# Kernel tuning notes

Measured on AMD Instinct MI355X. Metric: run time of the kernel, lower is better.

## Reference

```python
import jax, jax.numpy as jnp
import numpy as np

B, S, D = 1, 4096, 1024
H, W = 16, 512            # heads, window_size
HD = D // H               # head_dim = 64


def setup_inputs() -> dict:
    key = jax.random.key(0)
    k1, k2, k3 = jax.random.split(key, 3)
    x = jax.random.normal(k1, (B, S, D), dtype=jnp.float32)
    w_qkv = jax.random.normal(k2, (D, 3 * D), dtype=jnp.float32) * 0.02
    w_out = jax.random.normal(k3, (D, D), dtype=jnp.float32) * 0.02
    return {"x": x, "w_qkv": w_qkv, "w_out": w_out}


def reference(x, w_qkv, w_out):
    b, s, d = x.shape
    qkv = x @ w_qkv                                   # [B,S,3D]
    q, k, v = jnp.split(qkv, 3, axis=-1)
    to_heads = lambda t: t.reshape(b, s, H, HD).transpose(0, 2, 1, 3)  # [B,H,S,hd]
    q, k, v = map(to_heads, (q, k, v))

    C = s // W                                        # number of chunks
    qc = q.reshape(b, H, C, W, HD)                    # [B,H,C,W,hd]
    kc = k.reshape(b, H, C, W, HD)
    vc = v.reshape(b, H, C, W, HD)

    # each chunk attends to [previous chunk, current chunk] of K/V (2W keys)
    zero = jnp.zeros_like(kc[:, :, :1])
    k_prev = jnp.concatenate([zero, kc[:, :, :-1]], axis=2)
    v_prev = jnp.concatenate([jnp.zeros_like(vc[:, :, :1]), vc[:, :, :-1]], axis=2)
    kcat = jnp.concatenate([k_prev, kc], axis=3)      # [B,H,C,2W,hd]
    vcat = jnp.concatenate([v_prev, vc], axis=3)

    scores = jnp.einsum('bhcqd,bhckd->bhcqk', qc, kcat) / (HD ** 0.5)

    # mask: causal (abs q_pos >= abs k_pos) and k_pos >= 0 (first chunk has no prev)
    wq = jnp.arange(W)
    jk = jnp.arange(2 * W)
    ci = jnp.arange(C)
    causal = (wq[:, None] + W) >= jk[None, :]                    # [W,2W]
    valid = (ci[:, None, None] * W + jk[None, None, :] - W) >= 0  # [C,1,2W]
    mask = causal[None] & valid                                   # [C,W,2W]

    scores = jnp.where(mask[None, None], scores, -jnp.inf)
    attn = jax.nn.softmax(scores, axis=-1)
    out = jnp.einsum('bhcqk,bhckd->bhcqd', attn, vcat)            # [B,H,C,W,hd]
    out = out.reshape(b, H, s, HD).transpose(0, 2, 1, 3).reshape(b, s, d)
    return out @ w_out
```

## Files before the change

### kernel.cpp

```cpp
#include <hip/hip_runtime.h>

typedef __attribute__((ext_vector_type(8))) short short8;
typedef __attribute__((ext_vector_type(4))) float f32x4;
typedef __attribute__((ext_vector_type(4))) unsigned short us4;
typedef unsigned short u16;

__device__ __forceinline__ u16 f2bf(float f) {
  unsigned int u = __float_as_uint(f);
  u += 0x7fffu + ((u >> 16) & 1u);
  return (u16)(u >> 16);
}

__device__ __forceinline__ void gld16(const void* g, void* l) {
  __builtin_amdgcn_global_load_lds((const __attribute__((address_space(1))) void*)g,
                                   (__attribute__((address_space(3))) void*)l, 16, 0, 0);
}

__global__ __launch_bounds__(256) void cast_f32_to_bf16(const float* __restrict__ in,
                                                        u16* __restrict__ out, int n8) {
  int i = blockIdx.x * 256 + threadIdx.x;
  if (i >= n8) return;
  const f32x4* p = (const f32x4*)in;
  f32x4 a = p[i * 2];
  f32x4 b = p[i * 2 + 1];
  short8 o;
#pragma unroll
  for (int j = 0; j < 4; ++j) o[j] = (short)f2bf(a[j]);
#pragma unroll
  for (int j = 0; j < 4; ++j) o[4 + j] = (short)f2bf(b[j]);
  ((short8*)out)[i] = o;
}

__global__ __launch_bounds__(256) void transpose_cast(const float* __restrict__ w,
                                                      u16* __restrict__ wT, int K, int N) {
  __shared__ float tile[32][33];
  int n0 = blockIdx.x * 32, k0 = blockIdx.y * 32;
  int r = threadIdx.x >> 5;
  int c = threadIdx.x & 31;
#pragma unroll
  for (int i = 0; i < 4; ++i)
    tile[r + i * 8][c] = w[(size_t)(k0 + r + i * 8) * N + n0 + c];
  __syncthreads();
#pragma unroll
  for (int i = 0; i < 4; ++i)
    wT[(size_t)(n0 + r + i * 8) * K + k0 + c] = f2bf(tile[c][r + i * 8]);
}

__global__ __launch_bounds__(256) void transpose_v(const u16* __restrict__ vh,
                                                   u16* __restrict__ vt) {
  __shared__ u16 tile[32][33];
  const int s0 = blockIdx.x * 32, d0 = blockIdx.y * 32, h = blockIdx.z;
  const long hb = (long)h * 4096 * 64;
  const long hb2 = (long)h * 64 * 4096;
  const int r = threadIdx.x >> 5, c = threadIdx.x & 31;
#pragma unroll
  for (int i = 0; i < 4; ++i)
    tile[r + i * 8][c] = vh[hb + (long)(s0 + r + i * 8) * 64 + d0 + c];
  __syncthreads();
#pragma unroll
  for (int i = 0; i < 4; ++i)
    vt[hb2 + (long)(d0 + r + i * 8) * 4096 + s0 + c] = tile[c][r + i * 8];
}

template <int MODE, int BN>
__global__ __launch_bounds__(256) void gemm_bf16(
    const u16* __restrict__ A, const u16* __restrict__ Bt, float* __restrict__ C,
    u16* __restrict__ q_out, u16* __restrict__ k_out, u16* __restrict__ v_out,
    int M, int N, int K) {
  __shared__ __align__(16) u16 As[128][64];
  __shared__ __align__(16) u16 Bs[BN][64];
  constexpr int NW = BN / 32;
  const int t = threadIdx.x;
  const int lane = t & 63;
  const int wid = t >> 6;
  const int wm = wid >> 1, wn = wid & 1;
  const int l15 = lane & 15, lhi = lane >> 4;

  const int nbx = gridDim.x;
  const int bid = blockIdx.y * nbx + blockIdx.x;
  const int cpx = (nbx * gridDim.y) >> 3;
  const int wg = (bid & 7) * cpx + (bid >> 3);
  const int m0 = (wg / nbx) * 128;
  const int n0 = (wg % nbx) * BN;

  const int srow = lane >> 3;
  const int scol = ((lane & 7) ^ (lane >> 3)) * 8;

  f32x4 acc[4][NW];
#pragma unroll
  for (int mi = 0; mi < 4; ++mi)
#pragma unroll
    for (int ni = 0; ni < NW; ++ni) acc[mi][ni] = (f32x4){0.f, 0.f, 0.f, 0.f};

  for (int k0 = 0; k0 < K; k0 += 64) {
    __syncthreads();
#pragma unroll
    for (int i = 0; i < 4; ++i) {
      int cch = wid * 4 + i;
      int row = cch * 8 + srow;
      const u16* src = (MODE == 2)
          ? &A[((size_t)(k0 >> 6) * 4096 + m0 + row) * 64 + scol]
          : &A[(size_t)(m0 + row) * K + k0 + scol];
      gld16(src, &As[cch * 8][0]);
    }
#pragma unroll
    for (int i = 0; i < NW; ++i) {
      int cch = wid * NW + i;
      int row = cch * 8 + srow;
      gld16(&Bt[(size_t)(n0 + row) * K + k0 + scol], &Bs[cch * 8][0]);
    }
    __syncthreads();
#pragma unroll
    for (int kc = 0; kc < 2; ++kc) {
      short8 af[4], bf[NW];
#pragma unroll
      for (int mi = 0; mi < 4; ++mi) {
        int row = wm * 64 + mi * 16 + l15;
        af[mi] = *(const short8*)&As[row][((kc * 4 + lhi) ^ (l15 & 7)) * 8];
      }
#pragma unroll
      for (int ni = 0; ni < NW; ++ni) {
        int row = wn * (BN / 2) + ni * 16 + l15;
        bf[ni] = *(const short8*)&Bs[row][((kc * 4 + lhi) ^ (l15 & 7)) * 8];
      }
#pragma unroll
      for (int mi = 0; mi < 4; ++mi)
#pragma unroll
        for (int ni = 0; ni < NW; ++ni)
          acc[mi][ni] = __builtin_amdgcn_mfma_f32_16x16x32_bf16(af[mi], bf[ni], acc[mi][ni], 0, 0, 0);
    }
  }

  const float SCQ = 0.18033688011112042f;
#pragma unroll
  for (int mi = 0; mi < 4; ++mi)
#pragma unroll
    for (int ni = 0; ni < NW; ++ni)
#pragma unroll
      for (int r = 0; r < 4; ++r) {
        int row = m0 + wm * 64 + mi * 16 + lhi * 4 + r;
        int col = n0 + wn * (BN / 2) + ni * 16 + l15;
        float val = acc[mi][ni][r];
        if constexpr (MODE == 1) {
          int which = col >> 10;
          int d = col & 1023;
          int hh = d >> 6, hd = d & 63;
          if (which == 0)      q_out[((size_t)hh * 4096 + row) * 64 + hd] = f2bf(val * SCQ);
          else if (which == 1) k_out[((size_t)hh * 4096 + row) * 64 + hd] = f2bf(val);
          else                 v_out[((size_t)hh * 4096 + row) * 64 + hd] = f2bf(val);
        } else {
          C[(size_t)row * N + col] = val;
        }
      }
}

__global__ __launch_bounds__(256) void attn_kernel(
    const u16* __restrict__ qh,
    const u16* __restrict__ kh,
    const u16* __restrict__ vt,
    u16* __restrict__ outh) {
  __shared__ __align__(16) u16 Ks[2][64][64];
  __shared__ __align__(16) u16 Vt[2][64][64];
  __shared__ __align__(16) unsigned int Pl[4][32][37];

  const int t = threadIdx.x;
  const int lane = t & 63;
  const int w = t >> 6;
  const int l15 = lane & 15;
  const int lhi = lane >> 4;

  const int bid = blockIdx.x;
  const int wk = (bid & 7) * 64 + (bid >> 3);
  const int qt = wk & 3, c = (wk >> 2) & 7, h = wk >> 5;

  const long head_base = (long)h * 4096 * 64;
  const int q0 = qt * 128;
  const long q_gbase = head_base + (long)(c * 512 + q0) * 64;

  short8 qf[2][2];
#pragma unroll
  for (int mi = 0; mi < 2; ++mi)
#pragma unroll
    for (int kc = 0; kc < 2; ++kc)
      qf[mi][kc] = *(const short8*)&qh[q_gbase + (long)(w * 32 + mi * 16 + l15) * 64 + kc * 32 + lhi * 8];

  float m_run[2] = {-1e30f, -1e30f}, l_run[2] = {0.f, 0.f};
  f32x4 acc_o[2][4];
#pragma unroll
  for (int mi = 0; mi < 2; ++mi)
#pragma unroll
    for (int nd = 0; nd < 4; ++nd) acc_o[mi][nd] = (f32x4){0.f, 0.f, 0.f, 0.f};

  const int kt_start = (c == 0) ? 8 : 0;
  const int kt_end = 2 * qt + 9;
  const long kv_base = head_base + ((long)c - 1) * 512 * 64;
  const long vt_hb = (long)h * 64 * 4096 + ((long)c - 1) * 512;

  const int srow = lane >> 3;
  const int sunit8 = ((lane & 7) ^ (lane >> 3)) * 8;

  {
    const int j0 = kt_start * 64;
#pragma unroll
    for (int i = 0; i < 2; ++i) {
      int cch = w * 2 + i;
      gld16(&kh[kv_base + (long)(j0 + cch * 8 + srow) * 64 + sunit8], &Ks[0][cch * 8][0]);
      gld16(&vt[vt_hb + (long)(cch * 8 + srow) * 4096 + j0 + sunit8], &Vt[0][cch * 8][0]);
    }
  }
  __syncthreads();

  int cur = 0;
  for (int kt = kt_start; kt <= kt_end; ++kt) {
    const int j0 = kt * 64;
    const int nxt = cur ^ 1;

    if (kt < kt_end) {
      const int j0n = j0 + 64;
#pragma unroll
      for (int i = 0; i < 2; ++i) {
        int cch = w * 2 + i;
        gld16(&kh[kv_base + (long)(j0n + cch * 8 + srow) * 64 + sunit8], &Ks[nxt][cch * 8][0]);
        gld16(&vt[vt_hb + (long)(cch * 8 + srow) * 4096 + j0n + sunit8], &Vt[nxt][cch * 8][0]);
      }
    }

    const bool active = (j0 <= q0 + w * 32 + 31 + 512);
    if (active) {
      f32x4 sa[2][4];
#pragma unroll
      for (int mi = 0; mi < 2; ++mi)
#pragma unroll
        for (int ni = 0; ni < 4; ++ni) sa[mi][ni] = (f32x4){0.f, 0.f, 0.f, 0.f};
#pragma unroll
      for (int kc = 0; kc < 2; ++kc) {
        short8 kf[4];
#pragma unroll
        for (int ni = 0; ni < 4; ++ni) {
          int row = ni * 16 + l15;
          kf[ni] = *(const short8*)&Ks[cur][row][((kc * 4 + lhi) ^ (l15 & 7)) * 8];
        }
#pragma unroll
        for (int mi = 0; mi < 2; ++mi)
#pragma unroll
          for (int ni = 0; ni < 4; ++ni)
            sa[mi][ni] = __builtin_amdgcn_mfma_f32_16x16x32_bf16(kf[ni], qf[mi][kc], sa[mi][ni], 0, 0, 0);
      }

      const bool need_mask = (j0 + 63 > q0 + w * 32 + 512);
#pragma unroll
      for (int mi = 0; mi < 2; ++mi) {
        const int qloc = q0 + w * 32 + mi * 16 + l15;
        if (need_mask) {
          const int lim = qloc + 512 - j0 - 4 * lhi;
#pragma unroll
          for (int ni = 0; ni < 4; ++ni)
#pragma unroll
            for (int r = 0; r < 4; ++r)
              if (16 * ni + r > lim) sa[mi][ni][r] = -1e30f;
        }
        float v[16];
#pragma unroll
        for (int ni = 0; ni < 4; ++ni)
#pragma unroll
          for (int r = 0; r < 4; ++r) v[ni * 4 + r] = sa[mi][ni][r];
#pragma unroll
        for (int s = 8; s >= 1; s >>= 1)
#pragma unroll
          for (int k = 0; k < s; ++k) v[k] = fmaxf(v[k], v[k + s]);
        float tm = v[0];
        tm = fmaxf(tm, __shfl_xor(tm, 16, 64));
        tm = fmaxf(tm, __shfl_xor(tm, 32, 64));

        float mn = fmaxf(m_run[mi], tm);
        float corr = __builtin_amdgcn_exp2f(m_run[mi] - mn);
        m_run[mi] = mn;

        float ps[16];
#pragma unroll
        for (int ni = 0; ni < 4; ++ni) {
#pragma unroll
          for (int r = 0; r < 4; ++r) ps[ni * 4 + r] = __builtin_amdgcn_exp2f(sa[mi][ni][r] - mn);
          unsigned int p01 = (unsigned int)f2bf(ps[ni * 4 + 0]) | ((unsigned int)f2bf(ps[ni * 4 + 1]) << 16);
          unsigned int p23 = (unsigned int)f2bf(ps[ni * 4 + 2]) | ((unsigned int)f2bf(ps[ni * 4 + 3]) << 16);
          Pl[w][mi * 16 + l15][8 * ni + 2 * lhi + 0] = p01;
          Pl[w][mi * 16 + l15][8 * ni + 2 * lhi + 1] = p23;
        }
#pragma unroll
        for (int s = 8; s >= 1; s >>= 1)
#pragma unroll
          for (int k = 0; k < s; ++k) ps[k] += ps[k + s];
        float ls = ps[0];
        ls += __shfl_xor(ls, 16, 64);
        ls += __shfl_xor(ls, 32, 64);
        l_run[mi] = l_run[mi] * corr + ls;
#pragma unroll
        for (int nd = 0; nd < 4; ++nd)
#pragma unroll
          for (int r = 0; r < 4; ++r) acc_o[mi][nd][r] *= corr;
      }

#pragma unroll
      for (int kc = 0; kc < 2; ++kc) {
        short8 pf[2];
#pragma unroll
        for (int mi = 0; mi < 2; ++mi)
          pf[mi] = *(const short8*)&Pl[w][mi * 16 + l15][kc * 16 + lhi * 4];
#pragma unroll
        for (int nd = 0; nd < 4; ++nd) {
          int row = nd * 16 + l15;
          short8 vf = *(const short8*)&Vt[cur][row][((kc * 4 + lhi) ^ (l15 & 7)) * 8];
#pragma unroll
          for (int mi = 0; mi < 2; ++mi)
            acc_o[mi][nd] = __builtin_amdgcn_mfma_f32_16x16x32_bf16(vf, pf[mi], acc_o[mi][nd], 0, 0, 0);
        }
      }
    }
    __syncthreads();
    cur = nxt;
  }

#pragma unroll
  for (int mi = 0; mi < 2; ++mi) {
    float inv = 1.f / l_run[mi];
    long s = (long)c * 512 + q0 + w * 32 + mi * 16 + l15;
#pragma unroll
    for (int nd = 0; nd < 4; ++nd) {
      us4 o;
#pragma unroll
      for (int r = 0; r < 4; ++r) o[r] = f2bf(acc_o[mi][nd][r] * inv);
      *(us4*)&outh[head_base + s * 64 + nd * 16 + lhi * 4] = o;
    }
  }
}

extern "C" void kernel_launch(void* const* d_in, const int* in_sizes, int n_in,
                              void* d_out, int out_size, void* d_ws, size_t ws_size,
                              hipStream_t stream) {
  const float* x = (const float*)d_in[0];
  const float* w_qkv = (const float*)d_in[1];
  const float* w_out = (const float*)d_in[2];
  float* out = (float*)d_out;

  u16* xb = (u16*)d_ws;
  u16* wqkvT = xb + 4096 * 1024;
  u16* woutT = wqkvT + 3072 * 1024;
  u16* qh = woutT + 1024 * 1024;
  u16* kh = qh + 16 * 4096 * 64;
  u16* vh = kh + 16 * 4096 * 64;
  u16* vt = xb;

  cast_f32_to_bf16<<<2048, 256, 0, stream>>>(x, xb, 4096 * 1024 / 8);
  transpose_cast<<<dim3(96, 32), 256, 0, stream>>>(w_qkv, wqkvT, 1024, 3072);
  transpose_cast<<<dim3(32, 32), 256, 0, stream>>>(w_out, woutT, 1024, 1024);

  gemm_bf16<1, 128><<<dim3(24, 32), 256, 0, stream>>>(xb, wqkvT, nullptr, qh, kh, vh,
                                                      4096, 3072, 1024);
  transpose_v<<<dim3(128, 2, 16), 256, 0, stream>>>(vh, vt);
  attn_kernel<<<512, 256, 0, stream>>>(qh, kh, vt, qh);
  gemm_bf16<2, 64><<<dim3(16, 32), 256, 0, stream>>>(qh, woutT, out, nullptr, nullptr, nullptr,
                                                     4096, 1024, 1024);
}
```

Before: 182.5 us.

## Use 8 waves per attention block and smaller output GEMM tiles

The attention kernel now runs 512 threads per block, with each wave owning 16 query rows instead of 32. K/V tile loads are split across 8 waves, so each wave issues one load per tile instead of two. The output projection GEMM is templated on BM and uses 64x64 tiles, doubling the grid to fill more CUs. This lowers per-wave register pressure and raises parallelism, at the cost of less reuse of K/V fragments per MFMA and more per-wave softmax overhead.

```diff
diff --git a/kernel.cpp b/kernel.cpp
--- a/kernel.cpp
+++ b/kernel.cpp
@@ -62,13 +62,14 @@
     vt[hb2 + (long)(d0 + r + i * 8) * 4096 + s0 + c] = tile[c][r + i * 8];
 }
 
-template <int MODE, int BN>
+template <int MODE, int BM, int BN>
 __global__ __launch_bounds__(256) void gemm_bf16(
     const u16* __restrict__ A, const u16* __restrict__ Bt, float* __restrict__ C,
     u16* __restrict__ q_out, u16* __restrict__ k_out, u16* __restrict__ v_out,
     int M, int N, int K) {
-  __shared__ __align__(16) u16 As[128][64];
+  __shared__ __align__(16) u16 As[BM][64];
   __shared__ __align__(16) u16 Bs[BN][64];
+  constexpr int MW = BM / 32;
   constexpr int NW = BN / 32;
   const int t = threadIdx.x;
   const int lane = t & 63;
@@ -80,23 +81,23 @@
   const int bid = blockIdx.y * nbx + blockIdx.x;
   const int cpx = (nbx * gridDim.y) >> 3;
   const int wg = (bid & 7) * cpx + (bid >> 3);
-  const int m0 = (wg / nbx) * 128;
+  const int m0 = (wg / nbx) * BM;
   const int n0 = (wg % nbx) * BN;
 
   const int srow = lane >> 3;
   const int scol = ((lane & 7) ^ (lane >> 3)) * 8;
 
-  f32x4 acc[4][NW];
-#pragma unroll
-  for (int mi = 0; mi < 4; ++mi)
+  f32x4 acc[MW][NW];
+#pragma unroll
+  for (int mi = 0; mi < MW; ++mi)
 #pragma unroll
     for (int ni = 0; ni < NW; ++ni) acc[mi][ni] = (f32x4){0.f, 0.f, 0.f, 0.f};
 
   for (int k0 = 0; k0 < K; k0 += 64) {
     __syncthreads();
 #pragma unroll
-    for (int i = 0; i < 4; ++i) {
-      int cch = wid * 4 + i;
+    for (int i = 0; i < MW; ++i) {
+      int cch = wid * MW + i;
       int row = cch * 8 + srow;
       const u16* src = (MODE == 2)
           ? &A[((size_t)(k0 >> 6) * 4096 + m0 + row) * 64 + scol]
@@ -112,10 +113,10 @@
     __syncthreads();
 #pragma unroll
     for (int kc = 0; kc < 2; ++kc) {
-      short8 af[4], bf[NW];
-#pragma unroll
-      for (int mi = 0; mi < 4; ++mi) {
-        int row = wm * 64 + mi * 16 + l15;
+      short8 af[MW], bf[NW];
+#pragma unroll
+      for (int mi = 0; mi < MW; ++mi) {
+        int row = wm * (BM / 2) + mi * 16 + l15;
         af[mi] = *(const short8*)&As[row][((kc * 4 + lhi) ^ (l15 & 7)) * 8];
       }
 #pragma unroll
@@ -124,7 +125,7 @@
         bf[ni] = *(const short8*)&Bs[row][((kc * 4 + lhi) ^ (l15 & 7)) * 8];
       }
 #pragma unroll
-      for (int mi = 0; mi < 4; ++mi)
+      for (int mi = 0; mi < MW; ++mi)
 #pragma unroll
         for (int ni = 0; ni < NW; ++ni)
           acc[mi][ni] = __builtin_amdgcn_mfma_f32_16x16x32_bf16(af[mi], bf[ni], acc[mi][ni], 0, 0, 0);
@@ -133,12 +134,12 @@
 
   const float SCQ = 0.18033688011112042f;
 #pragma unroll
-  for (int mi = 0; mi < 4; ++mi)
+  for (int mi = 0; mi < MW; ++mi)
 #pragma unroll
     for (int ni = 0; ni < NW; ++ni)
 #pragma unroll
       for (int r = 0; r < 4; ++r) {
-        int row = m0 + wm * 64 + mi * 16 + lhi * 4 + r;
+        int row = m0 + wm * (BM / 2) + mi * 16 + lhi * 4 + r;
         int col = n0 + wn * (BN / 2) + ni * 16 + l15;
         float val = acc[mi][ni][r];
         if constexpr (MODE == 1) {
@@ -154,14 +155,14 @@
       }
 }
 
-__global__ __launch_bounds__(256) void attn_kernel(
+__global__ __launch_bounds__(512) void attn_kernel(
     const u16* __restrict__ qh,
     const u16* __restrict__ kh,
     const u16* __restrict__ vt,
     u16* __restrict__ outh) {
   __shared__ __align__(16) u16 Ks[2][64][64];
   __shared__ __align__(16) u16 Vt[2][64][64];
-  __shared__ __align__(16) unsigned int Pl[4][32][37];
+  __shared__ __align__(16) unsigned int Pl[8][16][37];
 
   const int t = threadIdx.x;
   const int lane = t & 63;
@@ -177,19 +178,15 @@
   const int q0 = qt * 128;
   const long q_gbase = head_base + (long)(c * 512 + q0) * 64;
 
-  short8 qf[2][2];
-#pragma unroll
-  for (int mi = 0; mi < 2; ++mi)
-#pragma unroll
-    for (int kc = 0; kc < 2; ++kc)
-      qf[mi][kc] = *(const short8*)&qh[q_gbase + (long)(w * 32 + mi * 16 + l15) * 64 + kc * 32 + lhi * 8];
-
-  float m_run[2] = {-1e30f, -1e30f}, l_run[2] = {0.f, 0.f};
-  f32x4 acc_o[2][4];
-#pragma unroll
-  for (int mi = 0; mi < 2; ++mi)
-#pragma unroll
-    for (int nd = 0; nd < 4; ++nd) acc_o[mi][nd] = (f32x4){0.f, 0.f, 0.f, 0.f};
+  short8 qf[2];
+#pragma unroll
+  for (int kc = 0; kc < 2; ++kc)
+    qf[kc] = *(const short8*)&qh[q_gbase + (long)(w * 16 + l15) * 64 + kc * 32 + lhi * 8];
+
+  float m_run = -1e30f, l_run = 0.f;
+  f32x4 acc_o[4];
+#pragma unroll
+  for (int nd = 0; nd < 4; ++nd) acc_o[nd] = (f32x4){0.f, 0.f, 0.f, 0.f};
 
   const int kt_start = (c == 0) ? 8 : 0;
   const int kt_end = 2 * qt + 9;
@@ -201,12 +198,8 @@
 
   {
     const int j0 = kt_start * 64;
-#pragma unroll
-    for (int i = 0; i < 2; ++i) {
-      int cch = w * 2 + i;
-      gld16(&kh[kv_base + (long)(j0 + cch * 8 + srow) * 64 + sunit8], &Ks[0][cch * 8][0]);
-      gld16(&vt[vt_hb + (long)(cch * 8 + srow) * 4096 + j0 + sunit8], &Vt[0][cch * 8][0]);
-    }
+    gld16(&kh[kv_base + (long)(j0 + w * 8 + srow) * 64 + sunit8], &Ks[0][w * 8][0]);
+    gld16(&vt[vt_hb + (long)(w * 8 + srow) * 4096 + j0 + sunit8], &Vt[0][w * 8][0]);
   }
   __syncthreads();
 
@@ -217,21 +210,15 @@
 
     if (kt < kt_end) {
       const int j0n = j0 + 64;
-#pragma unroll
-      for (int i = 0; i < 2; ++i) {
-        int cch = w * 2 + i;
-        gld16(&kh[kv_base + (long)(j0n + cch * 8 + srow) * 64 + sunit8], &Ks[nxt][cch * 8][0]);
-        gld16(&vt[vt_hb + (long)(cch * 8 + srow) * 4096 + j0n + sunit8], &Vt[nxt][cch * 8][0]);
-      }
-    }
-
-    const bool active = (j0 <= q0 + w * 32 + 31 + 512);
+      gld16(&kh[kv_base + (long)(j0n + w * 8 + srow) * 64 + sunit8], &Ks[nxt][w * 8][0]);
+      gld16(&vt[vt_hb + (long)(w * 8 + srow) * 4096 + j0n + sunit8], &Vt[nxt][w * 8][0]);
+    }
+
+    const bool active = (j0 <= q0 + w * 16 + 15 + 512);
     if (active) {
-      f32x4 sa[2][4];
-#pragma unroll
-      for (int mi = 0; mi < 2; ++mi)
-#pragma unroll
-        for (int ni = 0; ni < 4; ++ni) sa[mi][ni] = (f32x4){0.f, 0.f, 0.f, 0.f};
+      f32x4 sa[4];
+#pragma unroll
+      for (int ni = 0; ni < 4; ++ni) sa[ni] = (f32x4){0.f, 0.f, 0.f, 0.f};
 #pragma unroll
       for (int kc = 0; kc < 2; ++kc) {
         short8 kf[4];
@@ -241,78 +228,67 @@
           kf[ni] = *(const short8*)&Ks[cur][row][((kc * 4 + lhi) ^ (l15 & 7)) * 8];
         }
 #pragma unroll
-        for (int mi = 0; mi < 2; ++mi)
-#pragma unroll
-          for (int ni = 0; ni < 4; ++ni)
-            sa[mi][ni] = __builtin_amdgcn_mfma_f32_16x16x32_bf16(kf[ni], qf[mi][kc], sa[mi][ni], 0, 0, 0);
-      }
-
-      const bool need_mask = (j0 + 63 > q0 + w * 32 + 512);
-#pragma unroll
-      for (int mi = 0; mi < 2; ++mi) {
-        const int qloc = q0 + w * 32 + mi * 16 + l15;
-        if (need_mask) {
-          const int lim = qloc + 512 - j0 - 4 * lhi;
-#pragma unroll
-          for (int ni = 0; ni < 4; ++ni)
-#pragma unroll
-            for (int r = 0; r < 4; ++r)
-              if (16 * ni + r > lim) sa[mi][ni][r] = -1e30f;
-        }
-        float v[16];
-#pragma unroll
         for (int ni = 0; ni < 4; ++ni)
-#pragma unroll
-          for (int r = 0; r < 4; ++r) v[ni * 4 + r] = sa[mi][ni][r];
-#pragma unroll
-        for (int s = 8; s >= 1; s >>= 1)
-#pragma unroll
-          for (int k = 0; k < s; ++k) v[k] = fmaxf(v[k], v[k + s]);
-        float tm = v[0];
-        tm = fmaxf(tm, __shfl_xor(tm, 16, 64));
-        tm = fmaxf(tm, __shfl_xor(tm, 32, 64));
-
-        float mn = fmaxf(m_run[mi], tm);
-        float corr = __builtin_amdgcn_exp2f(m_run[mi] - mn);
-        m_run[mi] = mn;
-
-        float ps[16];
-#pragma unroll
-        for (int ni = 0; ni < 4; ++ni) {
-#pragma unroll
-          for (int r = 0; r < 4; ++r) ps[ni * 4 + r] = __builtin_amdgcn_exp2f(sa[mi][ni][r] - mn);
-          unsigned int p01 = (unsigned int)f2bf(ps[ni * 4 + 0]) | ((unsigned int)f2bf(ps[ni * 4 + 1]) << 16);
-          unsigned int p23 = (unsigned int)f2bf(ps[ni * 4 + 2]) | ((unsigned int)f2bf(ps[ni * 4 + 3]) << 16);
-          Pl[w][mi * 16 + l15][8 * ni + 2 * lhi + 0] = p01;
-          Pl[w][mi * 16 + l15][8 * ni + 2 * lhi + 1] = p23;
-        }
-#pragma unroll
-        for (int s = 8; s >= 1; s >>= 1)
-#pragma unroll
-          for (int k = 0; k < s; ++k) ps[k] += ps[k + s];
-        float ls = ps[0];
-        ls += __shfl_xor(ls, 16, 64);
-        ls += __shfl_xor(ls, 32, 64);
-        l_run[mi] = l_run[mi] * corr + ls;
-#pragma unroll
-        for (int nd = 0; nd < 4; ++nd)
-#pragma unroll
-          for (int r = 0; r < 4; ++r) acc_o[mi][nd][r] *= corr;
-      }
+          sa[ni] = __builtin_amdgcn_mfma_f32_16x16x32_bf16(kf[ni], qf[kc], sa[ni], 0, 0, 0);
+      }
+
+      const int qloc = q0 + w * 16 + l15;
+      if (j0 + 63 > q0 + w * 16 + 512) {
+        const int lim = qloc + 512 - j0 - 4 * lhi;
+#pragma unroll
+        for (int ni = 0; ni < 4; ++ni)
+#pragma unroll
+          for (int r = 0; r < 4; ++r)
+            if (16 * ni + r > lim) sa[ni][r] = -1e30f;
+      }
+      float v[16];
+#pragma unroll
+      for (int ni = 0; ni < 4; ++ni)
+#pragma unroll
+        for (int r = 0; r < 4; ++r) v[ni * 4 + r] = sa[ni][r];
+#pragma unroll
+      for (int s = 8; s >= 1; s >>= 1)
+#pragma unroll
+        for (int k = 0; k < s; ++k) v[k] = fmaxf(v[k], v[k + s]);
+      float tm = v[0];
+      tm = fmaxf(tm, __shfl_xor(tm, 16, 64));
+      tm = fmaxf(tm, __shfl_xor(tm, 32, 64));
+
+      float mn = fmaxf(m_run, tm);
+      float corr = __builtin_amdgcn_exp2f(m_run - mn);
+      m_run = mn;
+
+      float ps[16];
+#pragma unroll
+      for (int ni = 0; ni < 4; ++ni) {
+#pragma unroll
+        for (int r = 0; r < 4; ++r) ps[ni * 4 + r] = __builtin_amdgcn_exp2f(sa[ni][r] - mn);
+        unsigned int p01 = (unsigned int)f2bf(ps[ni * 4 + 0]) | ((unsigned int)f2bf(ps[ni * 4 + 1]) << 16);
+        unsigned int p23 = (unsigned int)f2bf(ps[ni * 4 + 2]) | ((unsigned int)f2bf(ps[ni * 4 + 3]) << 16);
+        Pl[w][l15][8 * ni + 2 * lhi + 0] = p01;
+        Pl[w][l15][8 * ni + 2 * lhi + 1] = p23;
+      }
+#pragma unroll
+      for (int s = 8; s >= 1; s >>= 1)
+#pragma unroll
+        for (int k = 0; k < s; ++k) ps[k] += ps[k + s];
+      float ls = ps[0];
+      ls += __shfl_xor(ls, 16, 64);
+      ls += __shfl_xor(ls, 32, 64);
+      l_run = l_run * corr + ls;
+#pragma unroll
+      for (int nd = 0; nd < 4; ++nd)
+#pragma unroll
+        for (int r = 0; r < 4; ++r) acc_o[nd][r] *= corr;
 
 #pragma unroll
       for (int kc = 0; kc < 2; ++kc) {
-        short8 pf[2];
-#pragma unroll
-        for (int mi = 0; mi < 2; ++mi)
-          pf[mi] = *(const short8*)&Pl[w][mi * 16 + l15][kc * 16 + lhi * 4];
+        short8 pf = *(const short8*)&Pl[w][l15][kc * 16 + lhi * 4];
 #pragma unroll
         for (int nd = 0; nd < 4; ++nd) {
           int row = nd * 16 + l15;
           short8 vf = *(const short8*)&Vt[cur][row][((kc * 4 + lhi) ^ (l15 & 7)) * 8];
-#pragma unroll
-          for (int mi = 0; mi < 2; ++mi)
-            acc_o[mi][nd] = __builtin_amdgcn_mfma_f32_16x16x32_bf16(vf, pf[mi], acc_o[mi][nd], 0, 0, 0);
+          acc_o[nd] = __builtin_amdgcn_mfma_f32_16x16x32_bf16(vf, pf, acc_o[nd], 0, 0, 0);
         }
       }
     }
@@ -320,15 +296,14 @@
     cur = nxt;
   }
 
-#pragma unroll
-  for (int mi = 0; mi < 2; ++mi) {
-    float inv = 1.f / l_run[mi];
-    long s = (long)c * 512 + q0 + w * 32 + mi * 16 + l15;
+  {
+    float inv = 1.f / l_run;
+    long s = (long)c * 512 + q0 + w * 16 + l15;
 #pragma unroll
     for (int nd = 0; nd < 4; ++nd) {
       us4 o;
 #pragma unroll
-      for (int r = 0; r < 4; ++r) o[r] = f2bf(acc_o[mi][nd][r] * inv);
+      for (int r = 0; r < 4; ++r) o[r] = f2bf(acc_o[nd][r] * inv);
       *(us4*)&outh[head_base + s * 64 + nd * 16 + lhi * 4] = o;
     }
   }
@@ -354,10 +329,10 @@
   transpose_cast<<<dim3(96, 32), 256, 0, stream>>>(w_qkv, wqkvT, 1024, 3072);
   transpose_cast<<<dim3(32, 32), 256, 0, stream>>>(w_out, woutT, 1024, 1024);
 
-  gemm_bf16<1, 128><<<dim3(24, 32), 256, 0, stream>>>(xb, wqkvT, nullptr, qh, kh, vh,
-                                                      4096, 3072, 1024);
+  gemm_bf16<1, 128, 128><<<dim3(24, 32), 256, 0, stream>>>(xb, wqkvT, nullptr, qh, kh, vh,
+                                                           4096, 3072, 1024);
   transpose_v<<<dim3(128, 2, 16), 256, 0, stream>>>(vh, vt);
-  attn_kernel<<<512, 256, 0, stream>>>(qh, kh, vt, qh);
-  gemm_bf16<2, 64><<<dim3(16, 32), 256, 0, stream>>>(qh, woutT, out, nullptr, nullptr, nullptr,
-                                                     4096, 1024, 1024);
-}
+  attn_kernel<<<512, 512, 0, stream>>>(qh, kh, vt, qh);
+  gemm_bf16<2, 64, 64><<<dim3(16, 64), 256, 0, stream>>>(qh, woutT, out, nullptr, nullptr, nullptr,
+                                                         4096, 1024, 1024);
+}
```

After: 175.1 us. -4.1%, faster.
